# Kernel tuning notes

Hardware: AMD Instinct MI355X
Metric: run time of the kernel (lower is better)

Reference implementation:

```python
import jax, jax.numpy as jnp
import numpy as np

ROPE_THETA = 10000.0


def _rotate_half(x):
    # interleaved rotation: out[..., 2i] = -x[..., 2i+1], out[..., 2i+1] = x[..., 2i]
    x_even = x[..., ::2]
    x_odd = x[..., 1::2]
    return jnp.stack([-x_odd, x_even], axis=-1).reshape(x.shape)


def _rope_cos_sin(N, D, dtype):
    inv_freq = 1.0 / (ROPE_THETA ** (jnp.arange(0, D, 2, dtype=jnp.float32) / D))  # [D/2]
    angles = jnp.arange(N, dtype=jnp.float32)[:, None] * inv_freq[None, :]          # [N, D/2]
    angles = jnp.repeat(angles, 2, axis=-1)                                          # [N, D]
    cos = jnp.cos(angles).astype(dtype)[None, :, None, :]  # [1, N, 1, D]
    sin = jnp.sin(angles).astype(dtype)[None, :, None, :]
    return cos, sin


def setup_inputs() -> dict:
    key = jax.random.key(0)
    kq, kk, kv, km = jax.random.split(key, 4)
    B, N, H, D = 16, 1024, 8, 64
    xq = jax.random.normal(kq, (B, N, H, D), dtype=jnp.float32)
    xk = jax.random.normal(kk, (B, N, H, D), dtype=jnp.float32)
    xv = jax.random.normal(kv, (B, N, H, D), dtype=jnp.float32)
    vis_mask = jax.random.bernoulli(km, 0.8, (B, N))  # bool visibility mask per batch
    return {"xq": xq, "xk": xk, "xv": xv, "vis_mask": vis_mask}


def reference(xq, xk, xv, vis_mask):
    B, N, H, D = xq.shape
    sm_scale = 1.0 / np.sqrt(D).astype(np.float32)

    # RoPE (interleaved) on q and k
    cos, sin = _rope_cos_sin(N, D, xq.dtype)
    q = xq * cos + _rotate_half(xq) * sin
    k = xk * cos + _rotate_half(xk) * sin

    # masked full attention: scores [B, H, N, N]
    scores = jnp.einsum("bnhd,bmhd->bhnm", q, k) * sm_scale
    attn_mask = (vis_mask[:, None, :, None] & vis_mask[:, None, None, :])  # [B,1,N,N]
    scores = jnp.where(attn_mask, scores, -jnp.inf)
    p = jax.nn.softmax(scores, axis=-1)
    p = jnp.nan_to_num(p, nan=0.0)  # fully-masked rows -> zeros (matches fallback)
    out = jnp.einsum("bhnm,bmhd->bnhd", p, xv)
    return out
```

## Files before the change

kernel.cpp:

```cpp
#include <hip/hip_runtime.h>
#include <hip/hip_bf16.h>
#include <stdint.h>

#define Bb 16
#define Nn 1024
#define Hh 8
#define Dd 64

typedef unsigned short u16;
typedef float f32x4 __attribute__((ext_vector_type(4)));
typedef short short8 __attribute__((ext_vector_type(8)));

union U4S8 { uint4 u; short8 s; };
union BF2U { __hip_bfloat162 h; uint32_t u; };

__device__ __forceinline__ uint32_t f2bf(float f){
  union{float f;uint32_t i;} v; v.f=f;
  return (v.i + 0x7fffu + ((v.i>>16)&1u))>>16;
}

__device__ __forceinline__ f32x4 mfma16(short8 a, short8 b, f32x4 c){
  return __builtin_amdgcn_mfma_f32_16x16x32_bf16(a,b,c,0,0,0);
}

typedef __attribute__((address_space(3))) uint32_t lds_u32;
typedef const __attribute__((address_space(1))) uint32_t glb_u32;
__device__ __forceinline__ void gl_lds16(const u16* g, u16* l){
  __builtin_amdgcn_global_load_lds((glb_u32*)g, (lds_u32*)l, 16, 0, 0);
}

#define ROPE_K 0.41524101186092030f
#define QS 0.18033688011112042f
#define NEGBIG -1.0e30f

__global__ __launch_bounds__(256) void rope_table_kernel(float2* __restrict__ tab)
{
  int id = blockIdx.x*256 + threadIdx.x;
  int i = id >> 10, n = id & 1023;
  float inv = exp2f(-(float)i * ROPE_K);
  float sn, cs; sincosf((float)n * inv, &sn, &cs);
  tab[id] = make_float2(cs, sn);
}

template<int USE_TAB>
__global__ __launch_bounds__(256) void prepass_kernel(
    const float* __restrict__ xk, const float* __restrict__ xv,
    u16* __restrict__ Kf, u16* __restrict__ Vf,
    const float2* __restrict__ tab)
{
  const int tid = threadIdx.x;
  const int bid = blockIdx.x;
  const int nt = bid & 15, h = (bid>>4)&7, b = bid>>7;
  const size_t bh = (size_t)b*Hh + h;
  const size_t tile = (bh<<4) + nt;

  {
    int r = tid>>2, c = (tid&3)<<4;
    int n = (nt<<6) + r;
    const float4* g = (const float4*)(xk + ((((size_t)b*Nn + n)*Hh + h)<<6) + c);
    float4 a0=g[0],a1=g[1],a2=g[2],a3=g[3];
    float xx[16] = {a0.x,a0.y,a0.z,a0.w, a1.x,a1.y,a1.z,a1.w,
                    a2.x,a2.y,a2.z,a2.w, a3.x,a3.y,a3.z,a3.w};
    uint32_t w[8];
    #pragma unroll
    for (int j=0;j<8;++j){
      int ii = (c>>1)+j;
      float cs, sn;
      if (USE_TAB){
        float2 t = tab[(ii<<10)+n]; cs = t.x; sn = t.y;
      } else {
        float inv = exp2f(-(float)ii * ROPE_K);
        sincosf((float)n * inv, &sn, &cs);
      }
      float x0 = xx[2*j], x1 = xx[2*j+1];
      float q0 = x0*cs - x1*sn;
      float q1 = x1*cs + x0*sn;
      w[j] = f2bf(q0) | (f2bf(q1)<<16);
    }
    int kb = r>>4, l15 = r&15;
    int half = c>>5, qd = (c>>3)&3;
    u16* base = Kf + (tile<<12);
    int dest0 = (kb<<10) + (half<<9) + (qd<<7) + (l15<<3);
    *(uint4*)(base + dest0)       = make_uint4(w[0],w[1],w[2],w[3]);
    *(uint4*)(base + dest0 + 128) = make_uint4(w[4],w[5],w[6],w[7]);
  }

  {
    int k = tid&63, ds = (tid>>6)<<4;
    int n = (nt<<6) + k;
    int slot = (k&1) | (((k>>4)&3)<<1) | (((k>>2)&3)<<3) | (((k>>1)&1)<<5);
    int half = slot>>5, qd = (slot>>3)&3, j = slot&7;
    const float4* g = (const float4*)(xv + ((((size_t)b*Nn + n)*Hh + h)<<6) + ds);
    float4 a0=g[0],a1=g[1],a2=g[2],a3=g[3];
    float vv[16] = {a0.x,a0.y,a0.z,a0.w, a1.x,a1.y,a1.z,a1.w,
                    a2.x,a2.y,a2.z,a2.w, a3.x,a3.y,a3.z,a3.w};
    u16* base = Vf + (tile<<12);
    #pragma unroll
    for (int jj=0;jj<16;++jj){
      int d = ds + jj;
      int s = d>>4, l15v = d&15;
      base[(s<<10) + (half<<9) + (qd<<7) + (l15v<<3) + j] = (u16)f2bf(vv[jj]);
    }
  }
}

template<int USE_TAB>
__global__ __launch_bounds__(256,4) void attn8_kernel(
    const float* __restrict__ xq, const u16* __restrict__ Kf,
    const u16* __restrict__ Vf, const int* __restrict__ vis,
    const float2* __restrict__ tab, float* __restrict__ out)
{
  __shared__ u16 KV[2][2][4096];
  __shared__ float biasS[Nn];

  const int tid  = threadIdx.x;
  const int lane = tid & 63;
  const int wave = tid >> 6;
  const int l15  = lane & 15;
  const int quad = lane >> 4;

  const int bid = blockIdx.x;
  const int xcd = bid & 7;
  const int ix  = bid >> 3;
  const int bh_ = (xcd<<4) | (ix>>3);
  const int qt  = ix & 7;
  const int h   = bh_ & 7;
  const int b   = bh_ >> 3;
  const size_t bh = (size_t)bh_;
  const int qbase = qt<<7;

  const int* visb = vis + b*Nn;
  const u16* Kfb = Kf + (bh<<16);
  const u16* Vfb = Vf + (bh<<16);

  {
    int4 vi = *(const int4*)&visb[tid<<2];
    float4 bs;
    bs.x = vi.x ? 0.f : NEGBIG;
    bs.y = vi.y ? 0.f : NEGBIG;
    bs.z = vi.z ? 0.f : NEGBIG;
    bs.w = vi.w ? 0.f : NEGBIG;
    *(float4*)&biasS[tid<<2] = bs;
  }

  short8 qa[2][2];
  #pragma unroll
  for (int mb=0; mb<2; ++mb){
    int n = qbase + (wave<<5) + (mb<<4) + l15;
    const float* src = xq + ((((size_t)b*Nn + n)*Hh + h)<<6);
    #pragma unroll
    for (int half=0; half<2; ++half){
      int d0 = (half<<5) + (quad<<3);
      const float4* g = (const float4*)(src + d0);
      float4 u0 = g[0], u1 = g[1];
      float xx[8] = {u0.x,u0.y,u0.z,u0.w, u1.x,u1.y,u1.z,u1.w};
      uint32_t w[4];
      #pragma unroll
      for (int j=0;j<4;++j){
        int i2 = (d0>>1) + j;
        float cs, sn;
        if (USE_TAB){
          float2 t = tab[(i2<<10)+n]; cs = t.x; sn = t.y;
        } else {
          float inv = exp2f(-(float)i2 * ROPE_K);
          sincosf((float)n * inv, &sn, &cs);
        }
        float x0 = xx[2*j], x1 = xx[2*j+1];
        float q0 = (x0*cs - x1*sn)*QS;
        float q1 = (x1*cs + x0*sn)*QS;
        w[j] = f2bf(q0) | (f2bf(q1)<<16);
      }
      U4S8 t; t.u = make_uint4(w[0],w[1],w[2],w[3]);
      qa[mb][half] = t.s;
    }
  }

  U4S8 ones_u; ones_u.u = make_uint4(0x3F803F80u,0x3F803F80u,0x3F803F80u,0x3F803F80u);
  const short8 ones = ones_u.s;

  f32x4 acc[2][4];
  f32x4 l_acc[2];
  #pragma unroll
  for (int mb=0;mb<2;++mb){
    l_acc[mb] = (f32x4){0.f,0.f,0.f,0.f};
    #pragma unroll
    for (int s=0;s<4;++s) acc[mb][s] = (f32x4){0.f,0.f,0.f,0.f};
  }

  const int t8 = tid<<3;

  gl_lds16(Kfb + t8,        &KV[0][0][t8]);
  gl_lds16(Kfb + 2048 + t8, &KV[0][0][2048 + t8]);
  gl_lds16(Vfb + t8,        &KV[0][1][t8]);
  gl_lds16(Vfb + 2048 + t8, &KV[0][1][2048 + t8]);
  __syncthreads();

  for (int kt=0; kt<16; ++kt){
    const int cur = kt & 1;
    if (kt < 15){
      const u16* kg = Kfb + ((kt+1)<<12);
      const u16* vg = Vfb + ((kt+1)<<12);
      gl_lds16(kg + t8,        &KV[cur^1][0][t8]);
      gl_lds16(kg + 2048 + t8, &KV[cur^1][0][2048 + t8]);
      gl_lds16(vg + t8,        &KV[cur^1][1][t8]);
      gl_lds16(vg + 2048 + t8, &KV[cur^1][1][2048 + t8]);
    }

    uint32_t pk[4][2][2];
    #pragma unroll
    for (int kb=0;kb<4;++kb){
      short8 kf0 = *(const short8*)&KV[cur][0][(kb<<10) + (lane<<3)];
      short8 kf1 = *(const short8*)&KV[cur][0][(kb<<10) + 512 + (lane<<3)];
      f32x4 bias = *(const f32x4*)&biasS[(kt<<6)+(kb<<4)+(quad<<2)];
      #pragma unroll
      for (int mb=0;mb<2;++mb){
        f32x4 t = mfma16(kf0, qa[mb][0], bias);
        t = mfma16(kf1, qa[mb][1], t);
        float p0 = __builtin_amdgcn_exp2f(t.x);
        float p1 = __builtin_amdgcn_exp2f(t.y);
        float p2 = __builtin_amdgcn_exp2f(t.z);
        float p3 = __builtin_amdgcn_exp2f(t.w);
        BF2U e0; e0.h = __float22bfloat162_rn(make_float2(p0,p1));
        BF2U e1; e1.h = __float22bfloat162_rn(make_float2(p2,p3));
        pk[kb][0][mb] = e0.u;
        pk[kb][1][mb] = e1.u;
      }
    }

    short8 pa[2][2];
    #pragma unroll
    for (int mb=0;mb<2;++mb){
      U4S8 a0; a0.u = make_uint4(pk[0][0][mb], pk[1][0][mb], pk[2][0][mb], pk[3][0][mb]);
      U4S8 a1; a1.u = make_uint4(pk[0][1][mb], pk[1][1][mb], pk[2][1][mb], pk[3][1][mb]);
      pa[mb][0] = a0.s; pa[mb][1] = a1.s;
    }

    #pragma unroll
    for (int mb=0;mb<2;++mb){
      l_acc[mb] = mfma16(pa[mb][0], ones, l_acc[mb]);
      l_acc[mb] = mfma16(pa[mb][1], ones, l_acc[mb]);
    }
    #pragma unroll
    for (int s=0;s<4;++s){
      short8 vb0 = *(const short8*)&KV[cur][1][(s<<10) + (lane<<3)];
      short8 vb1 = *(const short8*)&KV[cur][1][(s<<10) + 512 + (lane<<3)];
      #pragma unroll
      for (int mb=0;mb<2;++mb){
        acc[mb][s] = mfma16(pa[mb][0], vb0, acc[mb][s]);
        acc[mb][s] = mfma16(pa[mb][1], vb1, acc[mb][s]);
      }
    }

    __syncthreads();
  }

  #pragma unroll
  for (int mb=0;mb<2;++mb){
    #pragma unroll
    for (int rr=0;rr<4;++rr){
      int qrow = qbase + (wave<<5) + (mb<<4) + (quad<<2) + rr;
      float lq = l_acc[mb][rr];
      float invl = (biasS[qrow] == 0.f && lq > 0.f) ? 1.f/lq : 0.f;
      float* ob = out + ((((size_t)b*Nn + qrow)*Hh + h)<<6);
      #pragma unroll
      for (int s=0;s<4;++s)
        ob[(s<<4)+l15] = acc[mb][s][rr]*invl;
    }
  }
}

__device__ __forceinline__ void stage_rope_row_fb(const float* __restrict__ src,
                                                  u16 (*dst)[72],
                                                  int n_global, int sr, int d0)
{
  const float4* g = (const float4*)src;
  float4 a0 = g[0], a1 = g[1], a2 = g[2], a3 = g[3];
  float xx[16] = {a0.x,a0.y,a0.z,a0.w, a1.x,a1.y,a1.z,a1.w,
                  a2.x,a2.y,a2.z,a2.w, a3.x,a3.y,a3.z,a3.w};
  uint32_t w[8];
  #pragma unroll
  for (int j=0;j<8;++j){
    int i = (d0>>1)+j;
    float inv = exp2f(-(float)i * ROPE_K);
    float ang = (float)n_global * inv;
    float sn, cs; sincosf(ang, &sn, &cs);
    float x0 = xx[2*j], x1 = xx[2*j+1];
    float q0 = x0*cs - x1*sn;
    float q1 = x1*cs + x0*sn;
    w[j] = f2bf(q0) | (f2bf(q1)<<16);
  }
  *(uint4*)&dst[sr][d0]   = make_uint4(w[0],w[1],w[2],w[3]);
  *(uint4*)&dst[sr][d0+8] = make_uint4(w[4],w[5],w[6],w[7]);
}

__global__ __launch_bounds__(256,2) void attn_fallback(
    const float* __restrict__ xq, const float* __restrict__ xk,
    const float* __restrict__ xv, const int* __restrict__ vis,
    float* __restrict__ out)
{
  __shared__ u16 Qs[64][72];
  __shared__ u16 Ks[64][72];
  __shared__ u16 Vt[64][72];
  __shared__ u16 Ps[4][16][72];
  __shared__ float viss[64];

  const int tid  = threadIdx.x;
  const int wave = tid >> 6;
  const int lane = tid & 63;
  const int l15  = lane & 15;
  const int quad = lane >> 4;

  const int bid = blockIdx.x;
  const int qt = bid & 15;
  const int h  = (bid >> 4) & 7;
  const int b  = bid >> 7;

  const int sr = tid >> 2;
  const int d0 = (tid & 3) << 4;

  {
    int ng = (qt<<6) + sr;
    const float* src = xq + ((((size_t)b*Nn + ng)*Hh + h)<<6) + d0;
    stage_rope_row_fb(src, Qs, ng, sr, d0);
  }
  __syncthreads();

  short8 qa0 = *(const short8*)&Qs[(wave<<4)+l15][quad<<3];
  short8 qa1 = *(const short8*)&Qs[(wave<<4)+l15][(quad<<3)+32];

  f32x4 acc[4];
  #pragma unroll
  for (int s=0;s<4;++s) acc[s] = (f32x4){0.f,0.f,0.f,0.f};
  float m_r[4], l_r[4];
  #pragma unroll
  for (int rr=0;rr<4;++rr){ m_r[rr] = -1e30f; l_r[rr] = 0.f; }

  for (int kt=0; kt<16; ++kt){
    __syncthreads();
    {
      int ng = (kt<<6) + sr;
      const float* src = xk + ((((size_t)b*Nn + ng)*Hh + h)<<6) + d0;
      stage_rope_row_fb(src, Ks, ng, sr, d0);
    }
    {
      int ng = (kt<<6) + sr;
      const float4* g = (const float4*)(xv + ((((size_t)b*Nn + ng)*Hh + h)<<6) + d0);
      float4 a0 = g[0], a1 = g[1], a2 = g[2], a3 = g[3];
      float vv16[16] = {a0.x,a0.y,a0.z,a0.w, a1.x,a1.y,a1.z,a1.w,
                        a2.x,a2.y,a2.z,a2.w, a3.x,a3.y,a3.z,a3.w};
      #pragma unroll
      for (int j=0;j<16;++j) Vt[d0+j][sr] = (u16)f2bf(vv16[j]);
    }
    if (tid < 64) viss[tid] = (vis[b*Nn + (kt<<6) + tid] != 0) ? 1.f : 0.f;
    __syncthreads();

    f32x4 s4[4];
    #pragma unroll
    for (int n=0;n<4;++n){
      short8 kb0 = *(const short8*)&Ks[(n<<4)+l15][quad<<3];
      short8 kb1 = *(const short8*)&Ks[(n<<4)+l15][(quad<<3)+32];
      f32x4 t = (f32x4){0.f,0.f,0.f,0.f};
      t = mfma16(qa0, kb0, t);
      t = mfma16(qa1, kb1, t);
      s4[n] = t;
    }
    float vv[4];
    #pragma unroll
    for (int n=0;n<4;++n) vv[n] = viss[(n<<4)+l15];

    float p[4][4];
    #pragma unroll
    for (int rr=0; rr<4; ++rr){
      float sc[4];
      #pragma unroll
      for (int n=0;n<4;++n) sc[n] = (vv[n] > 0.f) ? s4[n][rr]*0.125f : -1e30f;
      float tm = fmaxf(fmaxf(sc[0],sc[1]), fmaxf(sc[2],sc[3]));
      tm = fmaxf(tm, __shfl_xor(tm,1));
      tm = fmaxf(tm, __shfl_xor(tm,2));
      tm = fmaxf(tm, __shfl_xor(tm,4));
      tm = fmaxf(tm, __shfl_xor(tm,8));
      float mnew  = fmaxf(m_r[rr], tm);
      float alpha = __expf(m_r[rr] - mnew);
      m_r[rr] = mnew;
      float psum = 0.f;
      #pragma unroll
      for (int n=0;n<4;++n){
        float pv = (vv[n] > 0.f) ? __expf(sc[n] - mnew) : 0.f;
        p[n][rr] = pv; psum += pv;
      }
      l_r[rr] = l_r[rr]*alpha + psum;
      #pragma unroll
      for (int s=0;s<4;++s) acc[s][rr] *= alpha;
    }

    #pragma unroll
    for (int n=0;n<4;++n)
      #pragma unroll
      for (int rr=0;rr<4;++rr)
        Ps[wave][(quad<<2)+rr][(n<<4)+l15] = (u16)f2bf(p[n][rr]);
    asm volatile("s_waitcnt lgkmcnt(0)" ::: "memory");
    short8 pa0 = *(const short8*)&Ps[wave][l15][quad<<3];
    short8 pa1 = *(const short8*)&Ps[wave][l15][(quad<<3)+32];

    #pragma unroll
    for (int s=0;s<4;++s){
      short8 vb0 = *(const short8*)&Vt[(s<<4)+l15][quad<<3];
      short8 vb1 = *(const short8*)&Vt[(s<<4)+l15][(quad<<3)+32];
      acc[s] = mfma16(pa0, vb0, acc[s]);
      acc[s] = mfma16(pa1, vb1, acc[s]);
    }
  }

  #pragma unroll
  for (int rr=0;rr<4;++rr){
    float t = l_r[rr];
    t += __shfl_xor(t,1); t += __shfl_xor(t,2);
    t += __shfl_xor(t,4); t += __shfl_xor(t,8);
    int row = (qt<<6) + (wave<<4) + (quad<<2) + rr;
    int qv  = vis[b*Nn + row];
    float invl = (qv != 0 && t > 0.f) ? 1.f/t : 0.f;
    size_t obase = (((size_t)b*Nn + row)*Hh + h) << 6;
    #pragma unroll
    for (int s=0;s<4;++s)
      out[obase + (s<<4) + l15] = acc[s][rr]*invl;
  }
}

extern "C" void kernel_launch(void* const* d_in, const int* in_sizes, int n_in,
                              void* d_out, int out_size, void* d_ws, size_t ws_size,
                              hipStream_t stream)
{
  const float* xq = (const float*)d_in[0];
  const float* xk = (const float*)d_in[1];
  const float* xv = (const float*)d_in[2];
  const int* vis  = (const int*)d_in[3];
  float* out = (float*)d_out;

  const size_t kv_elems = (size_t)Bb*Hh*Nn*Dd;
  const size_t kv_bytes = kv_elems*sizeof(u16);
  const size_t need_kv  = 2*kv_bytes;
  const size_t tab_bytes = (size_t)32*1024*sizeof(float2);

  if (d_ws != nullptr && ws_size >= need_kv + tab_bytes){
    u16* Kf = (u16*)d_ws;
    u16* Vf = Kf + kv_elems;
    float2* tab = (float2*)((char*)d_ws + need_kv);
    rope_table_kernel<<<dim3(128), dim3(256), 0, stream>>>(tab);
    prepass_kernel<1><<<dim3(Bb*Hh*(Nn/64)), dim3(256), 0, stream>>>(xk, xv, Kf, Vf, tab);
    attn8_kernel<1><<<dim3(Bb*Hh*(Nn/128)), dim3(256), 0, stream>>>(xq, Kf, Vf, vis, tab, out);
  } else if (d_ws != nullptr && ws_size >= need_kv){
    u16* Kf = (u16*)d_ws;
    u16* Vf = Kf + kv_elems;
    prepass_kernel<0><<<dim3(Bb*Hh*(Nn/64)), dim3(256), 0, stream>>>(xk, xv, Kf, Vf, nullptr);
    attn8_kernel<0><<<dim3(Bb*Hh*(Nn/128)), dim3(256), 0, stream>>>(xq, Kf, Vf, vis, nullptr, out);
  } else {
    attn_fallback<<<dim3(Bb*Hh*(Nn/64)), dim3(256), 0, stream>>>(xq, xk, xv, vis, out);
  }
}
```

Baseline: 189.6 us.

## Transpose RoPE table, stage prepass writes via LDS, add wave priority hints

The RoPE cos/sin table is laid out position-major so that each thread's lookups over frequency index are contiguous. The prepass now builds the K and V fragment tiles in shared memory and writes them to global memory with coalesced 16-byte stores, replacing the scattered 2-byte V stores. The attention loop raises wave priority around the MFMA sections with s_setprio to favour matrix issue. The prepass gains 16KB of LDS and a barrier.

```diff
diff --git a/kernel.cpp b/kernel.cpp
--- a/kernel.cpp
+++ b/kernel.cpp
@@ -36,7 +36,7 @@
 __global__ __launch_bounds__(256) void rope_table_kernel(float2* __restrict__ tab)
 {
   int id = blockIdx.x*256 + threadIdx.x;
-  int i = id >> 10, n = id & 1023;
+  int n = id >> 5, i = id & 31;
   float inv = exp2f(-(float)i * ROPE_K);
   float sn, cs; sincosf((float)n * inv, &sn, &cs);
   tab[id] = make_float2(cs, sn);
@@ -48,6 +48,9 @@
     u16* __restrict__ Kf, u16* __restrict__ Vf,
     const float2* __restrict__ tab)
 {
+  __shared__ u16 Kt[4096];
+  __shared__ u16 Vt[4096];
+
   const int tid = threadIdx.x;
   const int bid = blockIdx.x;
   const int nt = bid & 15, h = (bid>>4)&7, b = bid>>7;
@@ -67,7 +70,7 @@
       int ii = (c>>1)+j;
       float cs, sn;
       if (USE_TAB){
-        float2 t = tab[(ii<<10)+n]; cs = t.x; sn = t.y;
+        float2 t = tab[(n<<5)+ii]; cs = t.x; sn = t.y;
       } else {
         float inv = exp2f(-(float)ii * ROPE_K);
         sincosf((float)n * inv, &sn, &cs);
@@ -79,10 +82,9 @@
     }
     int kb = r>>4, l15 = r&15;
     int half = c>>5, qd = (c>>3)&3;
-    u16* base = Kf + (tile<<12);
     int dest0 = (kb<<10) + (half<<9) + (qd<<7) + (l15<<3);
-    *(uint4*)(base + dest0)       = make_uint4(w[0],w[1],w[2],w[3]);
-    *(uint4*)(base + dest0 + 128) = make_uint4(w[4],w[5],w[6],w[7]);
+    *(uint4*)&Kt[dest0]       = make_uint4(w[0],w[1],w[2],w[3]);
+    *(uint4*)&Kt[dest0 + 128] = make_uint4(w[4],w[5],w[6],w[7]);
   }
 
   {
@@ -94,13 +96,25 @@
     float4 a0=g[0],a1=g[1],a2=g[2],a3=g[3];
     float vv[16] = {a0.x,a0.y,a0.z,a0.w, a1.x,a1.y,a1.z,a1.w,
                     a2.x,a2.y,a2.z,a2.w, a3.x,a3.y,a3.z,a3.w};
-    u16* base = Vf + (tile<<12);
     #pragma unroll
     for (int jj=0;jj<16;++jj){
       int d = ds + jj;
       int s = d>>4, l15v = d&15;
-      base[(s<<10) + (half<<9) + (qd<<7) + (l15v<<3) + j] = (u16)f2bf(vv[jj]);
-    }
+      Vt[(s<<10) + (half<<9) + (qd<<7) + (l15v<<3) + j] = (u16)f2bf(vv[jj]);
+    }
+  }
+
+  __syncthreads();
+
+  {
+    const uint4* ks = (const uint4*)Kt;
+    const uint4* vs = (const uint4*)Vt;
+    uint4* kd = (uint4*)(Kf + (tile<<12));
+    uint4* vd = (uint4*)(Vf + (tile<<12));
+    kd[tid]       = ks[tid];
+    kd[tid + 256] = ks[tid + 256];
+    vd[tid]       = vs[tid];
+    vd[tid + 256] = vs[tid + 256];
   }
 }
 
@@ -160,7 +174,7 @@
         int i2 = (d0>>1) + j;
         float cs, sn;
         if (USE_TAB){
-          float2 t = tab[(i2<<10)+n]; cs = t.x; sn = t.y;
+          float2 t = tab[(n<<5)+i2]; cs = t.x; sn = t.y;
         } else {
           float inv = exp2f(-(float)i2 * ROPE_K);
           sincosf((float)n * inv, &sn, &cs);
@@ -207,6 +221,7 @@
     }
 
     uint32_t pk[4][2][2];
+    __builtin_amdgcn_s_setprio(1);
     #pragma unroll
     for (int kb=0;kb<4;++kb){
       short8 kf0 = *(const short8*)&KV[cur][0][(kb<<10) + (lane<<3)];
@@ -226,6 +241,7 @@
         pk[kb][1][mb] = e1.u;
       }
     }
+    __builtin_amdgcn_s_setprio(0);
 
     short8 pa[2][2];
     #pragma unroll
@@ -235,6 +251,7 @@
       pa[mb][0] = a0.s; pa[mb][1] = a1.s;
     }
 
+    __builtin_amdgcn_s_setprio(1);
     #pragma unroll
     for (int mb=0;mb<2;++mb){
       l_acc[mb] = mfma16(pa[mb][0], ones, l_acc[mb]);
@@ -250,6 +267,7 @@
         acc[mb][s] = mfma16(pa[mb][1], vb1, acc[mb][s]);
       }
     }
+    __builtin_amdgcn_s_setprio(0);
 
     __syncthreads();
   }
```

After: 176.0 us. 7.2% less time.
